# Kernel optimization log

Measured on AMD Instinct MI355X. Metric: run time of the kernel, lower is better.

The kernel has to match this reference:

```python
import jax, jax.numpy as jnp
import numpy as np

B, E, T = 8192, 512, 32


def setup_inputs() -> dict:
    key = jax.random.key(0)
    k1, k2, k3, k4, k5, k6 = jax.random.split(key, 6)
    s1 = 1.0 / np.sqrt(E)  # torch nn.Linear default init scale (uniform bound)
    return {
        "g_exp": jax.random.normal(k1, (B, E), dtype=jnp.float32),
        "tissue_vector": jax.random.randint(k2, (B, 1), 0, T, dtype=jnp.int64),
        # per-tissue head params: Linear(E,E) then Linear(E,1)
        "W1": jax.random.uniform(k3, (T, E, E), jnp.float32, -s1, s1),
        "b1": jax.random.uniform(k4, (T, E), jnp.float32, -s1, s1),
        "W2": jax.random.uniform(k5, (T, E), jnp.float32, -s1, s1),
        "b2": jax.random.uniform(k6, (T,), jnp.float32, -s1, s1),
    }


def reference(g_exp, tissue_vector, W1, b1, W2, b2):
    # Each sample b is routed through the MLP head of its tissue id.
    # Vectorized: run every sample through every tissue head, then select.
    # h[b,t,:] = GELU(g_exp[b] @ W1[t] + b1[t])
    h = jax.nn.gelu(jnp.einsum("be,teh->bth", g_exp, W1) + b1[None, :, :],
                    approximate=False)  # exact erf GELU, matches torch nn.GELU
    # y[b,t] = softplus(h[b,t] @ W2[t] + b2[t])   (Softplus since loss_fn='poisson')
    y = jax.nn.softplus(jnp.einsum("bth,th->bt", h, W2) + b2[None, :])
    tid = tissue_vector[:, 0]  # [B], tissue id per sample
    return jnp.take_along_axis(y, tid[:, None], axis=1)  # [B, 1]
```

## Files before the change

kernel.cpp:

```cpp
#include <hip/hip_runtime.h>
#include <hip/hip_bf16.h>
#include <math.h>

#define B_N 8192
#define E_N 512
#define T_N 32
#define BP 520

typedef short bf16x8 __attribute__((ext_vector_type(8)));
typedef float f32x4 __attribute__((ext_vector_type(4)));

#define WS_OFFS   256
#define WS_RANK   512
#define WS_ORDER  33280
#define WS_YACC   66048
#define WS_YACC8  98816
#define WS_REQ    (WS_YACC8 + 8 * B_N * 4)

static __device__ __forceinline__ unsigned short f2bf(float f) {
    unsigned int u = __float_as_uint(f);
    unsigned int r = u + 0x7fffu + ((u >> 16) & 1u);
    return (unsigned short)(r >> 16);
}

static __device__ __forceinline__ unsigned int pk2(float a, float b) {
    __hip_bfloat162 h = __float22bfloat162_rn(float2{a, b});
    unsigned int u;
    __builtin_memcpy(&u, &h, 4);
    return u;
}

__global__ __launch_bounds__(512, 4) void k_gemm_mfma(
    const float* __restrict__ g_exp, const float* __restrict__ W1,
    const int* __restrict__ tv, const float* __restrict__ b1,
    const float* __restrict__ W2, float* __restrict__ yacc8) {
    int wi = blockIdx.x;
    int t = wi & 31, nt = (wi >> 5) & 7, h = wi >> 8;
    int n0 = nt * 64;

    int tid = threadIdx.x;
    int w = tid >> 6, lane = tid & 63;
    int quad = (lane >> 4) & 3, l15 = lane & 15;

    __shared__ __align__(16) unsigned short Bs[64 * BP];
    __shared__ int rows_s[256];
    __shared__ int wsum[8];

    float b1v[4], w2v[4];
#pragma unroll
    for (int ni = 0; ni < 4; ++ni) {
        int n = t * E_N + n0 + ni * 16 + l15;
        b1v[ni] = b1[n];
        w2v[ni] = W2[n];
    }

    int tvals[16];
    const int4* tvp = (const int4*)(tv + tid * 16);
#pragma unroll
    for (int j = 0; j < 4; ++j) ((int4*)tvals)[j] = tvp[j];
    int myc = 0;
#pragma unroll
    for (int j = 0; j < 16; ++j) myc += (tvals[j] == t) ? 1 : 0;
    int inc = myc;
#pragma unroll
    for (int o = 1; o < 64; o <<= 1) {
        int u = __shfl_up(inc, o, 64);
        if (lane >= o) inc += u;
    }
    if (lane == 63) wsum[w] = inc;
    if (tid < 256) rows_s[tid] = 0;
    __syncthreads();
    int n_t = 0, wbase = 0;
#pragma unroll
    for (int i = 0; i < 8; ++i) {
        int v = wsum[i];
        n_t += v;
        if (i < w) wbase += v;
    }
    int nt_c = n_t > 512 ? 512 : n_t;
    int rk = wbase + inc - myc;
#pragma unroll
    for (int j = 0; j < 16; ++j)
        if (tvals[j] == t) {
            int rr = rk++;
            if (rr < 512 && (((rr >> 7) & 1) == h))
                rows_s[((rr >> 8) << 7) | (rr & 127)] = tid * 16 + j;
        }

    const float* Wsrc = W1 + (size_t)t * E_N * E_N + n0;
    unsigned int* Bw = (unsigned int*)Bs;
#pragma unroll 1
    for (int g = 0; g < 2; ++g) {
        float4 va[4], vb[4];
#pragma unroll
        for (int i = 0; i < 4; ++i) {
            int flat = (g * 4 + i) * 512 + tid;
            int k2 = flat >> 4, nq = flat & 15;
            va[i] = *(const float4*)(Wsrc + (size_t)(2 * k2) * E_N + nq * 4);
            vb[i] = *(const float4*)(Wsrc + (size_t)(2 * k2 + 1) * E_N + nq * 4);
        }
#pragma unroll
        for (int i = 0; i < 4; ++i) {
            int flat = (g * 4 + i) * 512 + tid;
            int k2 = flat >> 4, nq = flat & 15;
            int k2s = k2 ^ ((nq & 7) << 2);
            Bw[(nq * 4 + 0) * 260 + k2s] = pk2(va[i].x, vb[i].x);
            Bw[(nq * 4 + 1) * 260 + k2s] = pk2(va[i].y, vb[i].y);
            Bw[(nq * 4 + 2) * 260 + k2s] = pk2(va[i].z, vb[i].z);
            Bw[(nq * 4 + 3) * 260 + k2s] = pk2(va[i].w, vb[i].w);
        }
    }
    __syncthreads();

    int MCn = (nt_c + 127) >> 7;
    int MC = (MCn + 1 - h) >> 1;

    float* slab = yacc8 + (size_t)nt * B_N;

    for (int mc = 0; mc < MC; ++mc) {
        int row = rows_s[mc * 128 + w * 16 + l15];
        const f32x4* pA4 = (const f32x4*)(g_exp + (size_t)row * E_N) + quad * 2;

        f32x4 acc[4];
#pragma unroll
        for (int ni = 0; ni < 4; ++ni) acc[ni] = (f32x4){0.f, 0.f, 0.f, 0.f};

        f32x4 Alo0 = pA4[0],  Ahi0 = pA4[1];
        f32x4 Alo1 = pA4[8],  Ahi1 = pA4[9];
        f32x4 Alo2 = pA4[16], Ahi2 = pA4[17];
        f32x4 Alo3 = pA4[24], Ahi3 = pA4[25];

#define KSTEP(S, ks) do {                                                                   \
        unsigned int uu[4] = {pk2(Alo##S[0], Alo##S[1]), pk2(Alo##S[2], Alo##S[3]),         \
                              pk2(Ahi##S[0], Ahi##S[1]), pk2(Ahi##S[2], Ahi##S[3])};        \
        bf16x8 af;                                                                          \
        __builtin_memcpy(&af, uu, 16);                                                      \
        if (k4 < 3) {                                                                       \
            Alo##S = pA4[((ks) + 4) * 8];                                                   \
            Ahi##S = pA4[((ks) + 4) * 8 + 1];                                               \
        }                                                                                   \
        _Pragma("unroll") for (int ni = 0; ni < 4; ++ni) {                                  \
            int bswz = ((ni * 4 + (l15 >> 2)) & 7) << 3;        \
            bf16x8 bfr = *(const bf16x8*)(Bs + (ni * 16 + l15) * BP +                       \
                                          (((ks) * 32 + quad * 8) ^ bswz));                 \
            acc[ni] = __builtin_amdgcn_mfma_f32_16x16x32_bf16(af, bfr, acc[ni], 0, 0, 0);   \
        }                                                                                   \
    } while (0)

#pragma unroll 1
        for (int k4 = 0; k4 < 4; ++k4) {
            int ksb = k4 * 4;
            KSTEP(0, ksb + 0);
            KSTEP(1, ksb + 1);
            KSTEP(2, ksb + 2);
            KSTEP(3, ksb + 3);
        }
#undef KSTEP

        float pr[4] = {0.f, 0.f, 0.f, 0.f};
#pragma unroll
        for (int ni = 0; ni < 4; ++ni) {
#pragma unroll
            for (int r = 0; r < 4; ++r) {
                float u = acc[ni][r] + b1v[ni];
                float gg = 0.5f * u * (1.f + erff(u * 0.70710678118654752f));
                pr[r] = fmaf(gg, w2v[ni], pr[r]);
            }
        }
#pragma unroll
        for (int off = 1; off <= 8; off <<= 1)
#pragma unroll
            for (int r = 0; r < 4; ++r) pr[r] += __shfl_xor(pr[r], off, 64);

        if (l15 == 0) {
#pragma unroll
            for (int r = 0; r < 4; ++r) {
                int lidx = mc * 128 + w * 16 + quad * 4 + r;
                int grr = (2 * mc + h) * 128 + w * 16 + quad * 4 + r;
                if (grr < nt_c) slab[rows_s[lidx]] = pr[r];
            }
        }
    }
}

__global__ void k_final8(const float* __restrict__ yacc8, const int* __restrict__ tv,
                         const float* __restrict__ b2, float* __restrict__ out) {
    int b = blockIdx.x * blockDim.x + threadIdx.x;
    if (b < B_N) {
        float x = b2[tv[b]];
#pragma unroll
        for (int s = 0; s < 8; ++s) x += yacc8[(size_t)s * B_N + b];
        out[b] = fmaxf(x, 0.f) + log1pf(expf(-fabsf(x)));
    }
}

__global__ __launch_bounds__(256) void k_prep_sb(
    const int* __restrict__ tv, int* __restrict__ offs_g,
    int* __restrict__ rank, int* __restrict__ order, float* __restrict__ yacc) {
    __shared__ int lh[4][32], wcur[4][32], offs_s[33];
    int tid = threadIdx.x, w = tid >> 6;
    if (tid < 128) lh[tid >> 5][tid & 31] = 0;
    __syncthreads();
    int tval[32];
#pragma unroll
    for (int c = 0; c < 32; ++c) tval[c] = tv[c * 256 + tid];
#pragma unroll
    for (int c = 0; c < 32; ++c) atomicAdd(&lh[w][tval[c]], 1);
    __syncthreads();
    if (tid < 32) {
        int s = lh[0][tid] + lh[1][tid] + lh[2][tid] + lh[3][tid];
        int excl = 0;
#pragma unroll
        for (int i = 0; i < 32; ++i) {
            int v = __shfl(s, i, 64);
            if (i < tid) excl += v;
        }
        offs_s[tid] = excl;
        offs_g[tid] = excl;
        if (tid == 31) { offs_s[32] = excl + s; offs_g[32] = excl + s; }
    }
    __syncthreads();
    if (tid < 128) {
        int ww = tid >> 5, t = tid & 31;
        int s = offs_s[t];
        for (int w2 = 0; w2 < ww; ++w2) s += lh[w2][t];
        wcur[ww][t] = s;
    }
    __syncthreads();
#pragma unroll
    for (int c = 0; c < 32; ++c) {
        int b = c * 256 + tid;
        int pos = atomicAdd(&wcur[w][tval[c]], 1);
        rank[b] = pos;
        order[pos] = b;
    }
    float4 z = make_float4(0.f, 0.f, 0.f, 0.f);
#pragma unroll
    for (int c = 0; c < 8; ++c) *(float4*)(yacc + (c * 256 + tid) * 4) = z;
}

__global__ __launch_bounds__(256) void fb_gemm(
    const float* __restrict__ g_exp, const float* __restrict__ W1,
    const float* __restrict__ b1, const float* __restrict__ W2,
    const int* __restrict__ offs, const int* __restrict__ order,
    float* __restrict__ yacc) {
    int t = blockIdx.z;
    int base = offs[t];
    int n_t = offs[t + 1] - base;
    int m0 = blockIdx.y * 64;
    if (m0 >= n_t) return;
    int n0 = blockIdx.x * 128;

    __shared__ float As2[32][68];
    __shared__ float Bs2[32][128];
    __shared__ int sidx[64];

    int tid = threadIdx.x;
    if (tid < 64) {
        int m = m0 + tid;
        sidx[tid] = (m < n_t) ? order[base + m] : -1;
    }
    __syncthreads();

    int ty = tid >> 4, tx = tid & 15;
    float acc[4][8];
#pragma unroll
    for (int r = 0; r < 4; ++r)
#pragma unroll
        for (int c = 0; c < 8; ++c) acc[r][c] = 0.f;

    for (int k0 = 0; k0 < E_N; k0 += 32) {
#pragma unroll
        for (int p = 0; p < 2; ++p) {
            int idx = tid + 256 * p;
            int row = idx >> 3, kcq = idx & 7;
            int s = sidx[row];
            float4 v = make_float4(0.f, 0.f, 0.f, 0.f);
            if (s >= 0) v = *(const float4*)(g_exp + (size_t)s * E_N + k0 + kcq * 4);
            As2[kcq * 4 + 0][row] = v.x;
            As2[kcq * 4 + 1][row] = v.y;
            As2[kcq * 4 + 2][row] = v.z;
            As2[kcq * 4 + 3][row] = v.w;
        }
#pragma unroll
        for (int p = 0; p < 4; ++p) {
            int idx = tid + 256 * p;
            int kr = idx >> 5, c4 = idx & 31;
            *(float4*)(&Bs2[kr][c4 * 4]) =
                *(const float4*)(W1 + ((size_t)t * E_N + (k0 + kr)) * E_N + n0 + c4 * 4);
        }
        __syncthreads();
#pragma unroll
        for (int e = 0; e < 32; ++e) {
            float4 a = *(const float4*)(&As2[e][ty * 4]);
            float4 bA = *(const float4*)(&Bs2[e][tx * 4]);
            float4 bB = *(const float4*)(&Bs2[e][tx * 4 + 64]);
            float av[4] = {a.x, a.y, a.z, a.w};
            float bv[8] = {bA.x, bA.y, bA.z, bA.w, bB.x, bB.y, bB.z, bB.w};
#pragma unroll
            for (int r = 0; r < 4; ++r)
#pragma unroll
                for (int c = 0; c < 8; ++c) acc[r][c] = fmaf(av[r], bv[c], acc[r][c]);
        }
        __syncthreads();
    }

    float pr[4] = {0.f, 0.f, 0.f, 0.f};
#pragma unroll
    for (int c = 0; c < 8; ++c) {
        int n = n0 + tx * 4 + ((c >= 4) ? 64 : 0) + (c & 3);
        float bb = b1[t * E_N + n];
        float w2 = W2[t * E_N + n];
#pragma unroll
        for (int r = 0; r < 4; ++r) {
            float u = acc[r][c] + bb;
            float g = 0.5f * u * (1.f + erff(u * 0.70710678118654752f));
            pr[r] = fmaf(g, w2, pr[r]);
        }
    }
#pragma unroll
    for (int off = 8; off >= 1; off >>= 1)
#pragma unroll
        for (int r = 0; r < 4; ++r) pr[r] += __shfl_xor(pr[r], off, 64);

    if (tx == 0) {
#pragma unroll
        for (int r = 0; r < 4; ++r) {
            int m = m0 + ty * 4 + r;
            if (m < n_t) atomicAdd(&yacc[sidx[ty * 4 + r]], pr[r]);
        }
    }
}

__global__ void fb_final(const float* __restrict__ yacc, const int* __restrict__ tv,
                         const float* __restrict__ b2, float* __restrict__ out) {
    int b = blockIdx.x * blockDim.x + threadIdx.x;
    if (b < B_N) {
        float x = yacc[b] + b2[tv[b]];
        out[b] = fmaxf(x, 0.f) + log1pf(expf(-fabsf(x)));
    }
}

extern "C" void kernel_launch(void* const* d_in, const int* in_sizes, int n_in,
                              void* d_out, int out_size, void* d_ws, size_t ws_size,
                              hipStream_t stream) {
    const float* g_exp = (const float*)d_in[0];
    const int*   tv    = (const int*)d_in[1];
    const float* W1    = (const float*)d_in[2];
    const float* b1    = (const float*)d_in[3];
    const float* W2    = (const float*)d_in[4];
    const float* b2    = (const float*)d_in[5];
    float* out = (float*)d_out;

    char* ws = (char*)d_ws;

    if (ws_size >= (size_t)WS_REQ) {
        float* yacc8 = (float*)(ws + WS_YACC8);
        k_gemm_mfma<<<512, 512, 0, stream>>>(g_exp, W1, tv, b1, W2, yacc8);
        k_final8<<<32, 256, 0, stream>>>(yacc8, tv, b2, out);
    } else {
        int* offs   = (int*)(ws + WS_OFFS);
        int* rank   = (int*)(ws + WS_RANK);
        int* order  = (int*)(ws + WS_ORDER);
        float* yacc = (float*)(ws + WS_YACC);
        k_prep_sb<<<1, 256, 0, stream>>>(tv, offs, rank, order, yacc);
        fb_gemm<<<dim3(4, 8, 32), 256, 0, stream>>>(g_exp, W1, b1, W2, offs, order, yacc);
        fb_final<<<32, 256, 0, stream>>>(yacc, tv, b2, out);
    }
}
```

Before: 113.1 us.

## Pre-convert activations to bf16 and halve per-block N tile to 32

Adds a pre-pass kernel that converts g_exp to bf16 once into workspace, so the GEMM loads packed bf16 A fragments instead of fp32 values it must convert on every block. The GEMM's N tile shrinks from 64 to 32 columns, which doubles the grid to 1024 blocks, halves the LDS footprint and raises the occupancy hint to 8. The partial-sum slab count goes from 8 to 16 to match. In exchange there is an extra kernel launch, a larger workspace requirement, A rows re-read by twice as many blocks, and a heavier final reduction.

```diff
diff --git a/kernel.cpp b/kernel.cpp
--- a/kernel.cpp
+++ b/kernel.cpp
@@ -14,8 +14,9 @@
 #define WS_RANK   512
 #define WS_ORDER  33280
 #define WS_YACC   66048
-#define WS_YACC8  98816
-#define WS_REQ    (WS_YACC8 + 8 * B_N * 4)
+#define WS_YACC16 98816
+#define WS_GA     (WS_YACC16 + 16 * B_N * 4)
+#define WS_REQ    (WS_GA + (size_t)B_N * E_N * 2)
 
 static __device__ __forceinline__ unsigned short f2bf(float f) {
     unsigned int u = __float_as_uint(f);
@@ -30,25 +31,37 @@
     return u;
 }
 
-__global__ __launch_bounds__(512, 4) void k_gemm_mfma(
-    const float* __restrict__ g_exp, const float* __restrict__ W1,
+__global__ __launch_bounds__(256) void k_cvtA(const float* __restrict__ g_exp,
+                                              unsigned short* __restrict__ gA) {
+    int i = blockIdx.x * blockDim.x + threadIdx.x;
+    const f32x4* src = (const f32x4*)g_exp + (size_t)i * 2;
+    f32x4 a = src[0], b = src[1];
+    unsigned int uu[4] = {pk2(a[0], a[1]), pk2(a[2], a[3]),
+                          pk2(b[0], b[1]), pk2(b[2], b[3])};
+    int4 v;
+    __builtin_memcpy(&v, uu, 16);
+    *(int4*)(gA + (size_t)i * 8) = v;
+}
+
+__global__ __launch_bounds__(512, 8) void k_gemm_mfma(
+    const unsigned short* __restrict__ gA, const float* __restrict__ W1,
     const int* __restrict__ tv, const float* __restrict__ b1,
-    const float* __restrict__ W2, float* __restrict__ yacc8) {
+    const float* __restrict__ W2, float* __restrict__ yacc16) {
     int wi = blockIdx.x;
-    int t = wi & 31, nt = (wi >> 5) & 7, h = wi >> 8;
-    int n0 = nt * 64;
+    int t = wi & 31, nt = (wi >> 5) & 15, h = wi >> 9;
+    int n0 = nt * 32;
 
     int tid = threadIdx.x;
     int w = tid >> 6, lane = tid & 63;
     int quad = (lane >> 4) & 3, l15 = lane & 15;
 
-    __shared__ __align__(16) unsigned short Bs[64 * BP];
+    __shared__ __align__(16) unsigned short Bs[32 * BP];
     __shared__ int rows_s[256];
     __shared__ int wsum[8];
 
-    float b1v[4], w2v[4];
-#pragma unroll
-    for (int ni = 0; ni < 4; ++ni) {
+    float b1v[2], w2v[2];
+#pragma unroll
+    for (int ni = 0; ni < 2; ++ni) {
         int n = t * E_N + n0 + ni * 16 + l15;
         b1v[ni] = b1[n];
         w2v[ni] = W2[n];
@@ -89,20 +102,19 @@
 
     const float* Wsrc = W1 + (size_t)t * E_N * E_N + n0;
     unsigned int* Bw = (unsigned int*)Bs;
-#pragma unroll 1
-    for (int g = 0; g < 2; ++g) {
+    {
         float4 va[4], vb[4];
 #pragma unroll
         for (int i = 0; i < 4; ++i) {
-            int flat = (g * 4 + i) * 512 + tid;
-            int k2 = flat >> 4, nq = flat & 15;
+            int flat = i * 512 + tid;
+            int k2 = flat >> 3, nq = flat & 7;
             va[i] = *(const float4*)(Wsrc + (size_t)(2 * k2) * E_N + nq * 4);
             vb[i] = *(const float4*)(Wsrc + (size_t)(2 * k2 + 1) * E_N + nq * 4);
         }
 #pragma unroll
         for (int i = 0; i < 4; ++i) {
-            int flat = (g * 4 + i) * 512 + tid;
-            int k2 = flat >> 4, nq = flat & 15;
+            int flat = i * 512 + tid;
+            int k2 = flat >> 3, nq = flat & 7;
             int k2s = k2 ^ ((nq & 7) << 2);
             Bw[(nq * 4 + 0) * 260 + k2s] = pk2(va[i].x, vb[i].x);
             Bw[(nq * 4 + 1) * 260 + k2s] = pk2(va[i].y, vb[i].y);
@@ -115,31 +127,22 @@
     int MCn = (nt_c + 127) >> 7;
     int MC = (MCn + 1 - h) >> 1;
 
-    float* slab = yacc8 + (size_t)nt * B_N;
+    float* slab = yacc16 + (size_t)nt * B_N;
 
     for (int mc = 0; mc < MC; ++mc) {
         int row = rows_s[mc * 128 + w * 16 + l15];
-        const f32x4* pA4 = (const f32x4*)(g_exp + (size_t)row * E_N) + quad * 2;
-
-        f32x4 acc[4];
-#pragma unroll
-        for (int ni = 0; ni < 4; ++ni) acc[ni] = (f32x4){0.f, 0.f, 0.f, 0.f};
-
-        f32x4 Alo0 = pA4[0],  Ahi0 = pA4[1];
-        f32x4 Alo1 = pA4[8],  Ahi1 = pA4[9];
-        f32x4 Alo2 = pA4[16], Ahi2 = pA4[17];
-        f32x4 Alo3 = pA4[24], Ahi3 = pA4[25];
+        const bf16x8* pAb = (const bf16x8*)(gA + (size_t)row * E_N) + quad;
+
+        f32x4 acc[2];
+#pragma unroll
+        for (int ni = 0; ni < 2; ++ni) acc[ni] = (f32x4){0.f, 0.f, 0.f, 0.f};
+
+        bf16x8 A0 = pAb[0], A1 = pAb[4], A2 = pAb[8], A3 = pAb[12];
 
 #define KSTEP(S, ks) do {                                                                   \
-        unsigned int uu[4] = {pk2(Alo##S[0], Alo##S[1]), pk2(Alo##S[2], Alo##S[3]),         \
-                              pk2(Ahi##S[0], Ahi##S[1]), pk2(Ahi##S[2], Ahi##S[3])};        \
-        bf16x8 af;                                                                          \
-        __builtin_memcpy(&af, uu, 16);                                                      \
-        if (k4 < 3) {                                                                       \
-            Alo##S = pA4[((ks) + 4) * 8];                                                   \
-            Ahi##S = pA4[((ks) + 4) * 8 + 1];                                               \
-        }                                                                                   \
-        _Pragma("unroll") for (int ni = 0; ni < 4; ++ni) {                                  \
+        bf16x8 af = A##S;                                                                   \
+        if (k4 < 3) A##S = pAb[((ks) + 4) * 4];                                             \
+        _Pragma("unroll") for (int ni = 0; ni < 2; ++ni) {                                  \
             int bswz = ((ni * 4 + (l15 >> 2)) & 7) << 3;        \
             bf16x8 bfr = *(const bf16x8*)(Bs + (ni * 16 + l15) * BP +                       \
                                           (((ks) * 32 + quad * 8) ^ bswz));                 \
@@ -159,7 +162,7 @@
 
         float pr[4] = {0.f, 0.f, 0.f, 0.f};
 #pragma unroll
-        for (int ni = 0; ni < 4; ++ni) {
+        for (int ni = 0; ni < 2; ++ni) {
 #pragma unroll
             for (int r = 0; r < 4; ++r) {
                 float u = acc[ni][r] + b1v[ni];
@@ -183,13 +186,13 @@
     }
 }
 
-__global__ void k_final8(const float* __restrict__ yacc8, const int* __restrict__ tv,
-                         const float* __restrict__ b2, float* __restrict__ out) {
+__global__ void k_final16(const float* __restrict__ yacc16, const int* __restrict__ tv,
+                          const float* __restrict__ b2, float* __restrict__ out) {
     int b = blockIdx.x * blockDim.x + threadIdx.x;
     if (b < B_N) {
         float x = b2[tv[b]];
 #pragma unroll
-        for (int s = 0; s < 8; ++s) x += yacc8[(size_t)s * B_N + b];
+        for (int s = 0; s < 16; ++s) x += yacc16[(size_t)s * B_N + b];
         out[b] = fmaxf(x, 0.f) + log1pf(expf(-fabsf(x)));
     }
 }
@@ -355,9 +358,11 @@
     char* ws = (char*)d_ws;
 
     if (ws_size >= (size_t)WS_REQ) {
-        float* yacc8 = (float*)(ws + WS_YACC8);
-        k_gemm_mfma<<<512, 512, 0, stream>>>(g_exp, W1, tv, b1, W2, yacc8);
-        k_final8<<<32, 256, 0, stream>>>(yacc8, tv, b2, out);
+        float* yacc16 = (float*)(ws + WS_YACC16);
+        unsigned short* gA = (unsigned short*)(ws + WS_GA);
+        k_cvtA<<<(B_N * E_N / 8) / 256, 256, 0, stream>>>(g_exp, gA);
+        k_gemm_mfma<<<1024, 512, 0, stream>>>(gA, W1, tv, b1, W2, yacc16);
+        k_final16<<<32, 256, 0, stream>>>(yacc16, tv, b2, out);
     } else {
         int* offs   = (int*)(ws + WS_OFFS);
         int* rank   = (int*)(ws + WS_RANK);
```

After: 116.6 us. 1.03x slower.

## Precompute bf16 activations and tissue ordering; fuse final softplus into GEMM

Applied to the files above, without the earlier changes.

Adds a prep kernel that converts g_exp to bf16 once and builds a global counting-sort order of samples by tissue. The GEMM kernel no longer recomputes per-block tissue ranks and reads half-width bf16 activations directly. The separate final kernel is replaced by a last-block-done atomic counter inside the GEMM kernel. In exchange it adds an extra kernel pass over g_exp, needs more workspace, and serialises the final reduction onto a single block.

```diff
diff --git a/kernel.cpp b/kernel.cpp
--- a/kernel.cpp
+++ b/kernel.cpp
@@ -10,12 +10,14 @@
 typedef short bf16x8 __attribute__((ext_vector_type(8)));
 typedef float f32x4 __attribute__((ext_vector_type(4)));
 
+#define WS_CNT    128
 #define WS_OFFS   256
 #define WS_RANK   512
 #define WS_ORDER  33280
 #define WS_YACC   66048
 #define WS_YACC8  98816
-#define WS_REQ    (WS_YACC8 + 8 * B_N * 4)
+#define WS_GA     (WS_YACC8 + 8 * B_N * 4)
+#define WS_REQ    (WS_GA + (size_t)B_N * E_N * 2)
 
 static __device__ __forceinline__ unsigned short f2bf(float f) {
     unsigned int u = __float_as_uint(f);
@@ -30,10 +32,69 @@
     return u;
 }
 
+__global__ __launch_bounds__(256) void k_prep_cvt(
+    const float* __restrict__ g_exp, unsigned short* __restrict__ gA,
+    const int* __restrict__ tv, int* __restrict__ offs_g,
+    int* __restrict__ order, int* __restrict__ cnt) {
+    int blk = blockIdx.x;
+    int tid = threadIdx.x;
+    if (blk < 2048) {
+        int i = blk * 256 + tid;
+        const f32x4* src = (const f32x4*)g_exp + (size_t)i * 2;
+        f32x4 a = src[0], b = src[1];
+        unsigned int uu[4] = {pk2(a[0], a[1]), pk2(a[2], a[3]),
+                              pk2(b[0], b[1]), pk2(b[2], b[3])};
+        int4 v;
+        __builtin_memcpy(&v, uu, 16);
+        *(int4*)(gA + (size_t)i * 8) = v;
+        return;
+    }
+    __shared__ int lh[4][32], wcur[4][32], offs_s[33];
+    int w = tid >> 6;
+    if (tid < 128) lh[tid >> 5][tid & 31] = 0;
+    __syncthreads();
+    int tval[32];
+#pragma unroll
+    for (int c = 0; c < 32; ++c) tval[c] = tv[c * 256 + tid];
+#pragma unroll
+    for (int c = 0; c < 32; ++c) atomicAdd(&lh[w][tval[c]], 1);
+    __syncthreads();
+    if (tid < 32) {
+        int s = lh[0][tid] + lh[1][tid] + lh[2][tid] + lh[3][tid];
+        int excl = 0;
+#pragma unroll
+        for (int i = 0; i < 32; ++i) {
+            int v = __shfl(s, i, 64);
+            if (i < tid) excl += v;
+        }
+        offs_s[tid] = excl;
+        offs_g[tid] = excl;
+        if (tid == 31) { offs_s[32] = excl + s; offs_g[32] = excl + s; }
+    }
+    __syncthreads();
+    if (tid < 128) {
+        int ww = tid >> 5, t = tid & 31;
+        int s = offs_s[t];
+        for (int w2 = 0; w2 < ww; ++w2) s += lh[w2][t];
+        wcur[ww][t] = s;
+    }
+    __syncthreads();
+#pragma unroll
+    for (int c = 0; c < 32; ++c) {
+        int b = c * 256 + tid;
+        int pos = atomicAdd(&wcur[w][tval[c]], 1);
+        order[pos] = b;
+    }
+    if (tid == 0) *cnt = 0;
+}
+
 __global__ __launch_bounds__(512, 4) void k_gemm_mfma(
-    const float* __restrict__ g_exp, const float* __restrict__ W1,
-    const int* __restrict__ tv, const float* __restrict__ b1,
-    const float* __restrict__ W2, float* __restrict__ yacc8) {
+    const unsigned short* __restrict__ gA, const float* __restrict__ W1,
+    const int* __restrict__ offs, const int* __restrict__ order,
+    const float* __restrict__ b1, const float* __restrict__ W2,
+    float* __restrict__ yacc8, int* __restrict__ cnt,
+    const int* __restrict__ tv, const float* __restrict__ b2,
+    float* __restrict__ out) {
     int wi = blockIdx.x;
     int t = wi & 31, nt = (wi >> 5) & 7, h = wi >> 8;
     int n0 = nt * 64;
@@ -43,8 +104,9 @@
     int quad = (lane >> 4) & 3, l15 = lane & 15;
 
     __shared__ __align__(16) unsigned short Bs[64 * BP];
-    __shared__ int rows_s[256];
-    __shared__ int wsum[8];
+
+    int base = offs[t];
+    int n_t = offs[t + 1] - base;
 
     float b1v[4], w2v[4];
 #pragma unroll
@@ -53,39 +115,6 @@
         b1v[ni] = b1[n];
         w2v[ni] = W2[n];
     }
-
-    int tvals[16];
-    const int4* tvp = (const int4*)(tv + tid * 16);
-#pragma unroll
-    for (int j = 0; j < 4; ++j) ((int4*)tvals)[j] = tvp[j];
-    int myc = 0;
-#pragma unroll
-    for (int j = 0; j < 16; ++j) myc += (tvals[j] == t) ? 1 : 0;
-    int inc = myc;
-#pragma unroll
-    for (int o = 1; o < 64; o <<= 1) {
-        int u = __shfl_up(inc, o, 64);
-        if (lane >= o) inc += u;
-    }
-    if (lane == 63) wsum[w] = inc;
-    if (tid < 256) rows_s[tid] = 0;
-    __syncthreads();
-    int n_t = 0, wbase = 0;
-#pragma unroll
-    for (int i = 0; i < 8; ++i) {
-        int v = wsum[i];
-        n_t += v;
-        if (i < w) wbase += v;
-    }
-    int nt_c = n_t > 512 ? 512 : n_t;
-    int rk = wbase + inc - myc;
-#pragma unroll
-    for (int j = 0; j < 16; ++j)
-        if (tvals[j] == t) {
-            int rr = rk++;
-            if (rr < 512 && (((rr >> 7) & 1) == h))
-                rows_s[((rr >> 8) << 7) | (rr & 127)] = tid * 16 + j;
-        }
 
     const float* Wsrc = W1 + (size_t)t * E_N * E_N + n0;
     unsigned int* Bw = (unsigned int*)Bs;
@@ -112,33 +141,25 @@
     }
     __syncthreads();
 
-    int MCn = (nt_c + 127) >> 7;
+    int MCn = (n_t + 127) >> 7;
     int MC = (MCn + 1 - h) >> 1;
 
     float* slab = yacc8 + (size_t)nt * B_N;
 
     for (int mc = 0; mc < MC; ++mc) {
-        int row = rows_s[mc * 128 + w * 16 + l15];
-        const f32x4* pA4 = (const f32x4*)(g_exp + (size_t)row * E_N) + quad * 2;
+        int ridx = (2 * mc + h) * 128 + w * 16 + l15;
+        int row = order[base + (ridx < n_t ? ridx : 0)];
+        const bf16x8* pAb = (const bf16x8*)(gA + (size_t)row * E_N) + quad;
 
         f32x4 acc[4];
 #pragma unroll
         for (int ni = 0; ni < 4; ++ni) acc[ni] = (f32x4){0.f, 0.f, 0.f, 0.f};
 
-        f32x4 Alo0 = pA4[0],  Ahi0 = pA4[1];
-        f32x4 Alo1 = pA4[8],  Ahi1 = pA4[9];
-        f32x4 Alo2 = pA4[16], Ahi2 = pA4[17];
-        f32x4 Alo3 = pA4[24], Ahi3 = pA4[25];
+        bf16x8 A0 = pAb[0], A1 = pAb[4], A2 = pAb[8], A3 = pAb[12];
 
 #define KSTEP(S, ks) do {                                                                   \
-        unsigned int uu[4] = {pk2(Alo##S[0], Alo##S[1]), pk2(Alo##S[2], Alo##S[3]),         \
-                              pk2(Ahi##S[0], Ahi##S[1]), pk2(Ahi##S[2], Ahi##S[3])};        \
-        bf16x8 af;                                                                          \
-        __builtin_memcpy(&af, uu, 16);                                                      \
-        if (k4 < 3) {                                                                       \
-            Alo##S = pA4[((ks) + 4) * 8];                                                   \
-            Ahi##S = pA4[((ks) + 4) * 8 + 1];                                               \
-        }                                                                                   \
+        bf16x8 af = A##S;                                                                   \
+        if (k4 < 3) A##S = pAb[((ks) + 4) * 4];                                             \
         _Pragma("unroll") for (int ni = 0; ni < 4; ++ni) {                                  \
             int bswz = ((ni * 4 + (l15 >> 2)) & 7) << 3;        \
             bf16x8 bfr = *(const bf16x8*)(Bs + (ni * 16 + l15) * BP +                       \
@@ -175,22 +196,25 @@
         if (l15 == 0) {
 #pragma unroll
             for (int r = 0; r < 4; ++r) {
-                int lidx = mc * 128 + w * 16 + quad * 4 + r;
-                int grr = (2 * mc + h) * 128 + w * 16 + quad * 4 + r;
-                if (grr < nt_c) slab[rows_s[lidx]] = pr[r];
+                int rr = (2 * mc + h) * 128 + w * 16 + quad * 4 + r;
+                if (rr < n_t) slab[order[base + rr]] = pr[r];
             }
         }
     }
-}
-
-__global__ void k_final8(const float* __restrict__ yacc8, const int* __restrict__ tv,
-                         const float* __restrict__ b2, float* __restrict__ out) {
-    int b = blockIdx.x * blockDim.x + threadIdx.x;
-    if (b < B_N) {
-        float x = b2[tv[b]];
-#pragma unroll
-        for (int s = 0; s < 8; ++s) x += yacc8[(size_t)s * B_N + b];
-        out[b] = fmaxf(x, 0.f) + log1pf(expf(-fabsf(x)));
+
+    __threadfence();
+    __syncthreads();
+    __shared__ int lastf;
+    if (tid == 0) lastf = (atomicAdd(cnt, 1) == (int)gridDim.x - 1);
+    __syncthreads();
+    if (lastf) {
+        __threadfence();
+        for (int i = tid; i < B_N; i += 512) {
+            float x = b2[tv[i]];
+#pragma unroll
+            for (int s = 0; s < 8; ++s) x += yacc8[(size_t)s * B_N + i];
+            out[i] = fmaxf(x, 0.f) + log1pf(expf(-fabsf(x)));
+        }
     }
 }
 
@@ -355,9 +379,14 @@
     char* ws = (char*)d_ws;
 
     if (ws_size >= (size_t)WS_REQ) {
+        int* cnt    = (int*)(ws + WS_CNT);
+        int* offs   = (int*)(ws + WS_OFFS);
+        int* order  = (int*)(ws + WS_ORDER);
         float* yacc8 = (float*)(ws + WS_YACC8);
-        k_gemm_mfma<<<512, 512, 0, stream>>>(g_exp, W1, tv, b1, W2, yacc8);
-        k_final8<<<32, 256, 0, stream>>>(yacc8, tv, b2, out);
+        unsigned short* gA = (unsigned short*)(ws + WS_GA);
+        k_prep_cvt<<<2049, 256, 0, stream>>>(g_exp, gA, tv, offs, order, cnt);
+        k_gemm_mfma<<<512, 512, 0, stream>>>(gA, W1, offs, order, b1, W2,
+                                             yacc8, cnt, tv, b2, out);
     } else {
         int* offs   = (int*)(ws + WS_OFFS);
         int* rank   = (int*)(ws + WS_RANK);
```

Result: slower. 205.9 us (+82.0%).
